# Optimization experiments

Hardware: AMD Instinct MI355X
Metric: run time of the kernel (lower is better)

## Reference

```python
import jax, jax.numpy as jnp
import numpy as np

B, T, DM = 4, 1024, 1024
H, NW = 16, 16
HD = DM // H  # 64


def _l2norm(x, eps=1e-12):
    n = jnp.sqrt(jnp.sum(x * x, axis=-1, keepdims=True))
    return x / jnp.maximum(n, eps)


def setup_inputs() -> dict:
    key = jax.random.key(0)
    ks = jax.random.split(key, 14)
    s = 0.02
    d = {
        "x": jax.random.normal(ks[0], (B, T, DM), jnp.float32),
        "Wqf": jax.random.normal(ks[1], (H * NW, DM), jnp.float32) * s,
        "bqf": jnp.zeros((H * NW,), jnp.float32),
        "Wkf": jax.random.normal(ks[2], (H * NW, DM), jnp.float32) * s,
        "bkf": jnp.zeros((H * NW,), jnp.float32),
        "Wqp": jax.random.normal(ks[3], (H * NW, DM), jnp.float32) * s,
        "bqp": jnp.zeros((H * NW,), jnp.float32),
        "Wkp": jax.random.normal(ks[4], (H * NW, DM), jnp.float32) * s,
        "bkp": jnp.zeros((H * NW,), jnp.float32),
        "Wv": jax.random.normal(ks[5], (DM, DM), jnp.float32) * s,
        "bv": jnp.zeros((DM,), jnp.float32),
        "Wo": jax.random.normal(ks[6], (DM, DM), jnp.float32) * s,
        "bo": jnp.zeros((DM,), jnp.float32),
        "inter_scale": jnp.ones((H, 1, 1), jnp.float32),
    }
    return d


def reference(x, Wqf, bqf, Wkf, bkf, Wqp, bqp, Wkp, bkp, Wv, bv, Wo, bo, inter_scale):
    b, t, c = x.shape
    # projections -> [b, H, t, NW]
    def proj(W, bb, w_last):
        return (x @ W.T + bb).reshape(b, t, H, w_last).transpose(0, 2, 1, 3)

    q_f = proj(Wqf, bqf, NW)
    k_f = proj(Wkf, bkf, NW)
    q_p = proj(Wqp, bqp, NW)
    k_p = proj(Wkp, bkp, NW)
    v = proj(Wv, bv, HD)  # [b,H,t,HD]

    t_pos = jnp.arange(t, dtype=x.dtype)[None, None, :, None]  # [1,1,t,1]
    q_waves = jnp.sin(q_f * t_pos + q_p)
    k_waves = jnp.sin(k_f * t_pos + k_p)

    scale_factor = NW ** 0.25
    q_norm = _l2norm(q_waves) * scale_factor
    k_norm = _l2norm(k_waves) * scale_factor

    # wave interference scores [b,H,t,t]
    interference = jnp.einsum('bhtw,bhsw->bhts', q_norm, k_norm)
    interference = interference * inter_scale  # broadcast [H,1,1]

    causal = jnp.tril(jnp.ones((t, t), dtype=bool))  # True = attended
    # elu_plus_one kernel; masked positions -> elu(-inf)+1 == 0
    attn = jnp.where(causal, jax.nn.elu(interference) + 1.0, 0.0)

    num_attended = jnp.arange(1, t + 1, dtype=x.dtype)[None, None, :, None]
    attn = attn / jnp.sqrt(num_attended)

    out = jnp.einsum('bhts,bhsd->bhtd', attn, v)  # [b,H,t,HD]
    out = out.transpose(0, 2, 1, 3).reshape(b, t, c)
    return out @ Wo.T + bo
```

## Files before the change

### kernel.cpp

```cpp
#include <hip/hip_runtime.h>
#include <math.h>

typedef __attribute__((ext_vector_type(8))) short bf16x8;
typedef __attribute__((ext_vector_type(4))) float f32x4;
typedef __attribute__((ext_vector_type(4))) int i32x4;

typedef __attribute__((address_space(3))) void lds_void;
typedef __attribute__((address_space(1))) const void glb_cvoid;

__device__ __forceinline__ unsigned short f32_to_bf16(float f) {
    unsigned u = __float_as_uint(f);
    unsigned r = (u + 0x7FFFu + ((u >> 16) & 1u)) >> 16;
    return (unsigned short)r;
}
__device__ __forceinline__ float bf16_to_f32(unsigned short h) {
    return __uint_as_float(((unsigned)h) << 16);
}

__global__ __launch_bounds__(256)
void split_bf16(const float* __restrict__ src, unsigned short* __restrict__ hi,
                unsigned short* __restrict__ lo, int n4)
{
    const int i = blockIdx.x * 256 + threadIdx.x;
    if (i >= n4) return;
    float4 v = *reinterpret_cast<const float4*>(src + (size_t)i * 4);
    ushort4 h;
    h.x = f32_to_bf16(v.x); h.y = f32_to_bf16(v.y);
    h.z = f32_to_bf16(v.z); h.w = f32_to_bf16(v.w);
    *reinterpret_cast<ushort4*>(hi + (size_t)i * 4) = h;
    if (lo) {
        ushort4 l;
        l.x = f32_to_bf16(v.x - bf16_to_f32(h.x));
        l.y = f32_to_bf16(v.y - bf16_to_f32(h.y));
        l.z = f32_to_bf16(v.z - bf16_to_f32(h.z));
        l.w = f32_to_bf16(v.w - bf16_to_f32(h.w));
        *reinterpret_cast<ushort4*>(lo + (size_t)i * 4) = l;
    }
}

__global__ __launch_bounds__(256)
void split4_bf16(const float* __restrict__ Wqf, const float* __restrict__ Wkf,
                 const float* __restrict__ Wqp, const float* __restrict__ Wkp,
                 unsigned short* __restrict__ WfH, unsigned short* __restrict__ WfL,
                 unsigned short* __restrict__ WpH)
{
    const int i = blockIdx.x * 256 + threadIdx.x;
    const int sel = i >> 16, j = i & 65535;
    const float* W = (sel == 0) ? Wqf : (sel == 1) ? Wkf : (sel == 2) ? Wqp : Wkp;
    float4 v = *reinterpret_cast<const float4*>(W + (size_t)j * 4);
    ushort4 h;
    h.x = f32_to_bf16(v.x); h.y = f32_to_bf16(v.y);
    h.z = f32_to_bf16(v.z); h.w = f32_to_bf16(v.w);
    const size_t o = (size_t)(sel & 1) * 262144 + (size_t)j * 4;
    if (sel < 2) {
        *reinterpret_cast<ushort4*>(WfH + o) = h;
        ushort4 l;
        l.x = f32_to_bf16(v.x - bf16_to_f32(h.x));
        l.y = f32_to_bf16(v.y - bf16_to_f32(h.y));
        l.z = f32_to_bf16(v.z - bf16_to_f32(h.z));
        l.w = f32_to_bf16(v.w - bf16_to_f32(h.w));
        *reinterpret_cast<ushort4*>(WfL + o) = l;
    } else {
        *reinterpret_cast<ushort4*>(WpH + o) = h;
    }
}

__device__ __forceinline__ void xcd_tiles(int& tm, int& tn) {
    const int L = blockIdx.x + gridDim.x * blockIdx.y;
    const int nbn = gridDim.x;
    const int q3 = L >> 3;
    tn = q3 % nbn;
    tm = (L & 7) + 8 * (q3 / nbn);
}

__global__ __launch_bounds__(256)
void freq_gemm_norm(const unsigned short* __restrict__ xh,
                    const unsigned short* __restrict__ xl,
                    const unsigned short* __restrict__ WfH,
                    const unsigned short* __restrict__ WfL,
                    const unsigned short* __restrict__ WpH,
                    const float* __restrict__ bqf, const float* __restrict__ bkf,
                    const float* __restrict__ bqp, const float* __restrict__ bkp,
                    unsigned short* __restrict__ qn, unsigned short* __restrict__ kn)
{
    __shared__ __attribute__((aligned(16))) unsigned short Al[32 * 64];
    __shared__ __attribute__((aligned(16))) unsigned short Bl[64 * 64];

    int tm, tn;
    xcd_tiles(tm, tn);
    const int bm = tm * 32, bn = tn * 64;

    const int tid = threadIdx.x;
    const int w = tid >> 6, l = tid & 63;
    const int wr = w >> 1, wc = w & 1;
    const int lr = l & 15, lg = l >> 4;
    const int r8 = l >> 3;
    const int c8 = l & 7;
    const int csw = (c8 ^ r8) << 3;

    f32x4 accF[2], accP[2];
#pragma unroll
    for (int j = 0; j < 2; j++)
#pragma unroll
        for (int r = 0; r < 4; r++) { accF[j][r] = 0.f; accP[j][r] = 0.f; }

    for (int t = 0; t < 64; ++t) {
        const int seg = t >> 4;
        const int kc = (t << 6) & 1023;
        const unsigned short* Aseg = (seg == 1) ? xl : xh;
        const unsigned short* Bseg = (seg <= 1) ? WfH : (seg == 2) ? WfL : WpH;

        __builtin_amdgcn_global_load_lds(
            (glb_cvoid*)(Aseg + (size_t)(bm + w * 8 + r8) * 1024 + kc + csw),
            (lds_void*)(&Al[(w * 8) * 64]), 16, 0, 0);
#pragma unroll
        for (int i = 0; i < 2; i++)
            __builtin_amdgcn_global_load_lds(
                (glb_cvoid*)(Bseg + (size_t)(bn + w * 16 + i * 8 + r8) * 1024 + kc + csw),
                (lds_void*)(&Bl[(w * 16 + i * 8) * 64]), 16, 0, 0);
        __syncthreads();

        bf16x8 af[2], bfr[2][2];
#pragma unroll
        for (int kk = 0; kk < 2; kk++) {
            af[kk] = *reinterpret_cast<const bf16x8*>(
                &Al[(wr * 16 + lr) * 64 + (((kk * 4 + lg) ^ (lr & 7)) << 3)]);
#pragma unroll
            for (int j = 0; j < 2; j++)
                bfr[j][kk] = *reinterpret_cast<const bf16x8*>(
                    &Bl[(wc * 32 + j * 16 + lr) * 64 + (((kk * 4 + lg) ^ (lr & 7)) << 3)]);
        }
        if (seg < 3) {
#pragma unroll
            for (int kk = 0; kk < 2; kk++)
#pragma unroll
                for (int j = 0; j < 2; j++)
                    accF[j] = __builtin_amdgcn_mfma_f32_16x16x32_bf16(
                        af[kk], bfr[j][kk], accF[j], 0, 0, 0);
        } else {
#pragma unroll
            for (int kk = 0; kk < 2; kk++)
#pragma unroll
                for (int j = 0; j < 2; j++)
                    accP[j] = __builtin_amdgcn_mfma_f32_16x16x32_bf16(
                        af[kk], bfr[j][kk], accP[j], 0, 0, 0);
        }
        __syncthreads();
    }

#pragma unroll
    for (int j = 0; j < 2; j++) {
        const int col = bn + wc * 32 + j * 16 + lr;
        const bool isQ = col < 256;
        const int c = col & 255;
        const float bf = isQ ? bqf[c] : bkf[c];
        const float bp = isQ ? bqp[c] : bkp[c];
        unsigned short* dst = isQ ? qn : kn;
        const int h = c >> 4, ww = c & 15;
#pragma unroll
        for (int r = 0; r < 4; r++) {
            const int row = bm + wr * 16 + lg * 4 + r;
            const int b = row >> 10, t = row & 1023;
            const float f = accF[j][r] + bf;
            const float p = accP[j][r] + bp;
            const float s = __sinf(fmaf(f, (float)t, p));
            float n2 = s * s;
#pragma unroll
            for (int off = 8; off >= 1; off >>= 1)
                n2 += __shfl_xor(n2, off);
            const float val = s * 2.0f / fmaxf(sqrtf(n2), 1e-12f);
            dst[((size_t)(b * 16 + h) * 1024 + t) * 16 + ww] = f32_to_bf16(val);
        }
    }
}

template <int MODE>
__global__ __launch_bounds__(256)
void mfma_gemm(const unsigned short* __restrict__ A0,
               const unsigned short* __restrict__ B0,
               const float* __restrict__ bias,
               float* __restrict__ outF, unsigned short* __restrict__ outH)
{
    __shared__ __attribute__((aligned(16))) unsigned short Al[64 * 64];
    __shared__ __attribute__((aligned(16))) unsigned short Bl[64 * 64];

    int tm, tn;
    xcd_tiles(tm, tn);
    const int bm = tm * 64, bn = tn * 64;

    const int tid = threadIdx.x;
    const int w = tid >> 6, l = tid & 63;
    const int wr = w >> 1, wc = w & 1;
    const int lr = l & 15, lg = l >> 4;
    const int r8 = l >> 3;
    const int c8 = l & 7;
    const int csw = (c8 ^ r8) << 3;

    f32x4 acc[2][2];
#pragma unroll
    for (int i = 0; i < 2; i++)
#pragma unroll
        for (int j = 0; j < 2; j++)
#pragma unroll
            for (int r = 0; r < 4; r++) acc[i][j][r] = 0.f;

    for (int t = 0; t < 16; ++t) {
        const int k0 = t << 6;
#pragma unroll
        for (int i = 0; i < 2; i++) {
            __builtin_amdgcn_global_load_lds(
                (glb_cvoid*)(A0 + (size_t)(bm + w * 16 + i * 8 + r8) * 1024 + k0 + csw),
                (lds_void*)(&Al[(w * 16 + i * 8) * 64]), 16, 0, 0);
            __builtin_amdgcn_global_load_lds(
                (glb_cvoid*)(B0 + (size_t)(bn + w * 16 + i * 8 + r8) * 1024 + k0 + csw),
                (lds_void*)(&Bl[(w * 16 + i * 8) * 64]), 16, 0, 0);
        }
        __syncthreads();

        bf16x8 af[2][2], bfr[2][2];
#pragma unroll
        for (int i = 0; i < 2; i++)
#pragma unroll
            for (int kk = 0; kk < 2; kk++) {
                af[i][kk] = *reinterpret_cast<const bf16x8*>(
                    &Al[(wr * 32 + i * 16 + lr) * 64 + (((kk * 4 + lg) ^ (lr & 7)) << 3)]);
                bfr[i][kk] = *reinterpret_cast<const bf16x8*>(
                    &Bl[(wc * 32 + i * 16 + lr) * 64 + (((kk * 4 + lg) ^ (lr & 7)) << 3)]);
            }
#pragma unroll
        for (int kk = 0; kk < 2; kk++)
#pragma unroll
            for (int i = 0; i < 2; i++)
#pragma unroll
                for (int j = 0; j < 2; j++)
                    acc[i][j] = __builtin_amdgcn_mfma_f32_16x16x32_bf16(
                        af[i][kk], bfr[j][kk], acc[i][j], 0, 0, 0);
        __syncthreads();
    }

#pragma unroll
    for (int i = 0; i < 2; i++) {
#pragma unroll
        for (int j = 0; j < 2; j++) {
#pragma unroll
            for (int r = 0; r < 4; r++) {
                const int row = bm + wr * 32 + i * 16 + lg * 4 + r;
                const int col = bn + wc * 32 + j * 16 + lr;
                float v = acc[i][j][r] + bias[col];
                if (MODE == 1) {
                    const int hh = col >> 6, d = col & 63;
                    const int b = row >> 10, t = row & 1023;
                    outH[(((size_t)(b * 16 + hh) * 64 + d) * 1024) + t] =
                        f32_to_bf16(v);
                } else {
                    outF[(size_t)row * 1024 + col] = v;
                }
            }
        }
    }
}

__global__ __launch_bounds__(512)
void wave_attn_mfma(const unsigned short* __restrict__ qn,
                    const unsigned short* __restrict__ kn,
                    const unsigned short* __restrict__ vtt,
                    const float* __restrict__ iscale,
                    unsigned short* __restrict__ y)
{
    const int p = blockIdx.x, bh = blockIdx.y;
    const int h = bh & 15, b = bh >> 4;
    const int tid = threadIdx.x;
    const int wq = tid >> 6;
    const int l = tid & 63;
    const int lt = l & 15;
    const int gl = l >> 4;
    const int it = (wq < 4) ? p : (15 - p);
    const int t0w = it * 64 + (wq & 3) * 16;
    const float scale = iscale[h];
    const int tmine = t0w + lt;

    const bf16x8 zero8 = {0, 0, 0, 0, 0, 0, 0, 0};
    const f32x4 zf = {0.f, 0.f, 0.f, 0.f};
    const size_t kb = (size_t)bh * 1024;

    bf16x8 bq = zero8;
    if (gl < 2)
        bq = *reinterpret_cast<const bf16x8*>(&qn[(kb + t0w + lt) * 16 + gl * 8]);

    f32x4 o[4];
#pragma unroll
    for (int jd = 0; jd < 4; jd++) o[jd] = zf;

    const int addr0 = ((2 * (gl & 1)) * 16 + lt) * 4;
    const int addr1 = addr0 + 64;
    const bool hi = ((gl >> 1) & 1) != 0;

    bf16x8 akc[4], akn[4];
#pragma unroll
    for (int js = 0; js < 4; js++) {
        akc[js] = zero8;
        if (gl < 2)
            akc[js] = *reinterpret_cast<const bf16x8*>(
                &kn[(kb + js * 16 + lt) * 16 + gl * 8]);
    }

    for (int is = 0; is <= it; is++) {
        const int s0 = is * 64;

        if (is < it) {
#pragma unroll
            for (int js = 0; js < 4; js++) {
                akn[js] = zero8;
                if (gl < 2)
                    akn[js] = *reinterpret_cast<const bf16x8*>(
                        &kn[(kb + s0 + 64 + js * 16 + lt) * 16 + gl * 8]);
            }
        }
        bf16x8 bv[2][4];
#pragma unroll
        for (int ks = 0; ks < 2; ks++)
#pragma unroll
            for (int jd = 0; jd < 4; jd++)
                bv[ks][jd] = *reinterpret_cast<const bf16x8*>(
                    &vtt[((size_t)(bh * 64 + jd * 16 + lt)) * 1024 +
                         s0 + ks * 32 + gl * 8]);

        f32x4 st[4];
#pragma unroll
        for (int js = 0; js < 4; js++)
            st[js] = __builtin_amdgcn_mfma_f32_16x16x32_bf16(
                akc[js], bq, zf, 0, 0, 0);

        int pk[4][2];
#pragma unroll
        for (int js = 0; js < 4; js++) {
            float pp[4];
#pragma unroll
            for (int r = 0; r < 4; r++) {
                const int s = s0 + js * 16 + gl * 4 + r;
                const float xv = st[js][r] * scale;
                const float phi = (xv > 0.f) ? (xv + 1.0f) : __expf(xv);
                pp[r] = (s <= tmine) ? phi : 0.f;
            }
            asm("v_cvt_pk_bf16_f32 %0, %1, %2"
                : "=v"(pk[js][0]) : "v"(pp[0]), "v"(pp[1]));
            asm("v_cvt_pk_bf16_f32 %0, %1, %2"
                : "=v"(pk[js][1]) : "v"(pp[2]), "v"(pp[3]));
        }

        int rg[4][2][2];
#pragma unroll
        for (int js = 0; js < 4; js++)
#pragma unroll
            for (int sl = 0; sl < 2; sl++) {
                rg[js][sl][0] = __builtin_amdgcn_ds_bpermute(addr0, pk[js][sl]);
                rg[js][sl][1] = __builtin_amdgcn_ds_bpermute(addr1, pk[js][sl]);
            }

#pragma unroll
        for (int ks = 0; ks < 2; ks++) {
            i32x4 au;
#pragma unroll
            for (int c = 0; c < 2; c++)
#pragma unroll
                for (int sl = 0; sl < 2; sl++)
                    au[2 * c + sl] = hi ? rg[2 * ks + 1][sl][c]
                                        : rg[2 * ks][sl][c];
            const bf16x8 pa = __builtin_bit_cast(bf16x8, au);
#pragma unroll
            for (int jd = 0; jd < 4; jd++)
                o[jd] = __builtin_amdgcn_mfma_f32_16x16x32_bf16(
                    pa, bv[ks][jd], o[jd], 0, 0, 0);
        }

#pragma unroll
        for (int js = 0; js < 4; js++) akc[js] = akn[js];
    }

#pragma unroll
    for (int r = 0; r < 4; r++) {
        const int t = t0w + gl * 4 + r;
        const float inv = rsqrtf((float)(t + 1));
#pragma unroll
        for (int jd = 0; jd < 4; jd++) {
            const int d = jd * 16 + lt;
            y[((size_t)b * 1024 + t) * 1024 + h * 64 + d] =
                f32_to_bf16(o[jd][r] * inv);
        }
    }
}

extern "C" void kernel_launch(void* const* d_in, const int* in_sizes, int n_in,
                              void* d_out, int out_size, void* d_ws, size_t ws_size,
                              hipStream_t stream)
{
    const float* x   = (const float*)d_in[0];
    const float* Wqf = (const float*)d_in[1];
    const float* bqf = (const float*)d_in[2];
    const float* Wkf = (const float*)d_in[3];
    const float* bkf = (const float*)d_in[4];
    const float* Wqp = (const float*)d_in[5];
    const float* bqp = (const float*)d_in[6];
    const float* Wkp = (const float*)d_in[7];
    const float* bkp = (const float*)d_in[8];
    const float* Wv  = (const float*)d_in[9];
    const float* bv  = (const float*)d_in[10];
    const float* Wo  = (const float*)d_in[11];
    const float* bo  = (const float*)d_in[12];
    const float* isc = (const float*)d_in[13];
    float* out = (float*)d_out;

    char* ws = (char*)d_ws;
    unsigned short* ybf = (unsigned short*)(ws);
    unsigned short* qn  = (unsigned short*)(ws + ( 8u << 20));
    unsigned short* kn  = (unsigned short*)(ws + (10u << 20));
    unsigned short* WfH = (unsigned short*)(ws + (12u << 20));
    unsigned short* WfL = (unsigned short*)(ws + (13u << 20));
    unsigned short* WpH = (unsigned short*)(ws + (14u << 20));
    unsigned short* xh  = (unsigned short*)(ws + (16u << 20));
    unsigned short* xl  = (unsigned short*)(ws + (24u << 20));
    unsigned short* vtt = (unsigned short*)(ws + (24u << 20));
    unsigned short* WvH = (unsigned short*)(ws + (32u << 20));
    unsigned short* WoH = WvH;

    split_bf16<<<4096, 256, 0, stream>>>(x, xh, xl, 1048576);
    split4_bf16<<<1024, 256, 0, stream>>>(Wqf, Wkf, Wqp, Wkp, WfH, WfL, WpH);

    freq_gemm_norm<<<dim3(8, 128), 256, 0, stream>>>(
        xh, xl, WfH, WfL, WpH, bqf, bkf, bqp, bkp, qn, kn);

    split_bf16<<<1024, 256, 0, stream>>>(Wv, WvH, nullptr, 262144);
    mfma_gemm<1><<<dim3(16, 64), 256, 0, stream>>>(xh, WvH, bv, nullptr, vtt);

    wave_attn_mfma<<<dim3(8, 64), 512, 0, stream>>>(qn, kn, vtt, isc, ybf);

    split_bf16<<<1024, 256, 0, stream>>>(Wo, WoH, nullptr, 262144);
    mfma_gemm<2><<<dim3(16, 64), 256, 0, stream>>>(ybf, WoH, bo, out, nullptr);
}
```

Before: 220.3 us.

## Load GEMM operands directly from global into registers and merge Wv/Wo conversion

Both GEMM kernels drop LDS staging (global_load_lds plus barriers) and have each lane read its MFMA fragments straight from global memory. Operands that were shared through LDS are now re-read per wave and served by the caches. This removes the barriers and LDS traffic but makes global loads uncoalesced, with 16-byte strided rows. Separately, the Wv and Wo bf16 conversions become one kernel launched early, which needs a separate WoH buffer.

```diff
diff --git a/kernel.cpp b/kernel.cpp
--- a/kernel.cpp
+++ b/kernel.cpp
@@ -4,9 +4,6 @@
 typedef __attribute__((ext_vector_type(8))) short bf16x8;
 typedef __attribute__((ext_vector_type(4))) float f32x4;
 typedef __attribute__((ext_vector_type(4))) int i32x4;
-
-typedef __attribute__((address_space(3))) void lds_void;
-typedef __attribute__((address_space(1))) const void glb_cvoid;
 
 __device__ __forceinline__ unsigned short f32_to_bf16(float f) {
     unsigned u = __float_as_uint(f);
@@ -65,6 +62,21 @@
     }
 }
 
+__global__ __launch_bounds__(256)
+void splitW2_bf16(const float* __restrict__ Wv, const float* __restrict__ Wo,
+                  unsigned short* __restrict__ WvH, unsigned short* __restrict__ WoH)
+{
+    const int i = blockIdx.x * 256 + threadIdx.x;
+    const int sel = i >> 18, j = i & 262143;
+    const float* W = sel ? Wo : Wv;
+    unsigned short* D = sel ? WoH : WvH;
+    float4 v = *reinterpret_cast<const float4*>(W + (size_t)j * 4);
+    ushort4 h;
+    h.x = f32_to_bf16(v.x); h.y = f32_to_bf16(v.y);
+    h.z = f32_to_bf16(v.z); h.w = f32_to_bf16(v.w);
+    *reinterpret_cast<ushort4*>(D + (size_t)j * 4) = h;
+}
+
 __device__ __forceinline__ void xcd_tiles(int& tm, int& tn) {
     const int L = blockIdx.x + gridDim.x * blockIdx.y;
     const int nbn = gridDim.x;
@@ -83,9 +95,6 @@
                     const float* __restrict__ bqp, const float* __restrict__ bkp,
                     unsigned short* __restrict__ qn, unsigned short* __restrict__ kn)
 {
-    __shared__ __attribute__((aligned(16))) unsigned short Al[32 * 64];
-    __shared__ __attribute__((aligned(16))) unsigned short Bl[64 * 64];
-
     int tm, tn;
     xcd_tiles(tm, tn);
     const int bm = tm * 32, bn = tn * 64;
@@ -94,9 +103,10 @@
     const int w = tid >> 6, l = tid & 63;
     const int wr = w >> 1, wc = w & 1;
     const int lr = l & 15, lg = l >> 4;
-    const int r8 = l >> 3;
-    const int c8 = l & 7;
-    const int csw = (c8 ^ r8) << 3;
+
+    const size_t aoff  = (size_t)(bm + wr * 16 + lr) * 1024 + lg * 8;
+    const size_t boff0 = (size_t)(bn + wc * 32 + lr) * 1024 + lg * 8;
+    const size_t boff1 = boff0 + 16 * 1024;
 
     f32x4 accF[2], accP[2];
 #pragma unroll
@@ -104,49 +114,26 @@
 #pragma unroll
         for (int r = 0; r < 4; r++) { accF[j][r] = 0.f; accP[j][r] = 0.f; }
 
-    for (int t = 0; t < 64; ++t) {
-        const int seg = t >> 4;
-        const int kc = (t << 6) & 1023;
-        const unsigned short* Aseg = (seg == 1) ? xl : xh;
-        const unsigned short* Bseg = (seg <= 1) ? WfH : (seg == 2) ? WfL : WpH;
-
-        __builtin_amdgcn_global_load_lds(
-            (glb_cvoid*)(Aseg + (size_t)(bm + w * 8 + r8) * 1024 + kc + csw),
-            (lds_void*)(&Al[(w * 8) * 64]), 16, 0, 0);
-#pragma unroll
-        for (int i = 0; i < 2; i++)
-            __builtin_amdgcn_global_load_lds(
-                (glb_cvoid*)(Bseg + (size_t)(bn + w * 16 + i * 8 + r8) * 1024 + kc + csw),
-                (lds_void*)(&Bl[(w * 16 + i * 8) * 64]), 16, 0, 0);
-        __syncthreads();
-
-        bf16x8 af[2], bfr[2][2];
-#pragma unroll
-        for (int kk = 0; kk < 2; kk++) {
-            af[kk] = *reinterpret_cast<const bf16x8*>(
-                &Al[(wr * 16 + lr) * 64 + (((kk * 4 + lg) ^ (lr & 7)) << 3)]);
-#pragma unroll
-            for (int j = 0; j < 2; j++)
-                bfr[j][kk] = *reinterpret_cast<const bf16x8*>(
-                    &Bl[(wc * 32 + j * 16 + lr) * 64 + (((kk * 4 + lg) ^ (lr & 7)) << 3)]);
-        }
-        if (seg < 3) {
-#pragma unroll
-            for (int kk = 0; kk < 2; kk++)
-#pragma unroll
-                for (int j = 0; j < 2; j++)
-                    accF[j] = __builtin_amdgcn_mfma_f32_16x16x32_bf16(
-                        af[kk], bfr[j][kk], accF[j], 0, 0, 0);
-        } else {
-#pragma unroll
-            for (int kk = 0; kk < 2; kk++)
-#pragma unroll
-                for (int j = 0; j < 2; j++)
-                    accP[j] = __builtin_amdgcn_mfma_f32_16x16x32_bf16(
-                        af[kk], bfr[j][kk], accP[j], 0, 0, 0);
-        }
-        __syncthreads();
-    }
+    auto run_seg = [&](const unsigned short* __restrict__ A,
+                       const unsigned short* __restrict__ B, f32x4* acc) {
+#pragma unroll 4
+        for (int t = 0; t < 16; ++t) {
+            const int kc = t << 6;
+#pragma unroll
+            for (int kk = 0; kk < 2; kk++) {
+                const int ko = kc + kk * 32;
+                bf16x8 a  = *reinterpret_cast<const bf16x8*>(A + aoff  + ko);
+                bf16x8 b0 = *reinterpret_cast<const bf16x8*>(B + boff0 + ko);
+                bf16x8 b1 = *reinterpret_cast<const bf16x8*>(B + boff1 + ko);
+                acc[0] = __builtin_amdgcn_mfma_f32_16x16x32_bf16(a, b0, acc[0], 0, 0, 0);
+                acc[1] = __builtin_amdgcn_mfma_f32_16x16x32_bf16(a, b1, acc[1], 0, 0, 0);
+            }
+        }
+    };
+    run_seg(xh, WfH, accF);
+    run_seg(xl, WfH, accF);
+    run_seg(xh, WfL, accF);
+    run_seg(xh, WpH, accP);
 
 #pragma unroll
     for (int j = 0; j < 2; j++) {
@@ -181,9 +168,6 @@
                const float* __restrict__ bias,
                float* __restrict__ outF, unsigned short* __restrict__ outH)
 {
-    __shared__ __attribute__((aligned(16))) unsigned short Al[64 * 64];
-    __shared__ __attribute__((aligned(16))) unsigned short Bl[64 * 64];
-
     int tm, tn;
     xcd_tiles(tm, tn);
     const int bm = tm * 64, bn = tn * 64;
@@ -192,9 +176,11 @@
     const int w = tid >> 6, l = tid & 63;
     const int wr = w >> 1, wc = w & 1;
     const int lr = l & 15, lg = l >> 4;
-    const int r8 = l >> 3;
-    const int c8 = l & 7;
-    const int csw = (c8 ^ r8) << 3;
+
+    const size_t a0off = (size_t)(bm + wr * 32 + lr) * 1024 + lg * 8;
+    const size_t a1off = a0off + 16 * 1024;
+    const size_t b0off = (size_t)(bn + wc * 32 + lr) * 1024 + lg * 8;
+    const size_t b1off = b0off + 16 * 1024;
 
     f32x4 acc[2][2];
 #pragma unroll
@@ -204,38 +190,21 @@
 #pragma unroll
             for (int r = 0; r < 4; r++) acc[i][j][r] = 0.f;
 
+#pragma unroll 2
     for (int t = 0; t < 16; ++t) {
-        const int k0 = t << 6;
-#pragma unroll
-        for (int i = 0; i < 2; i++) {
-            __builtin_amdgcn_global_load_lds(
-                (glb_cvoid*)(A0 + (size_t)(bm + w * 16 + i * 8 + r8) * 1024 + k0 + csw),
-                (lds_void*)(&Al[(w * 16 + i * 8) * 64]), 16, 0, 0);
-            __builtin_amdgcn_global_load_lds(
-                (glb_cvoid*)(B0 + (size_t)(bn + w * 16 + i * 8 + r8) * 1024 + k0 + csw),
-                (lds_void*)(&Bl[(w * 16 + i * 8) * 64]), 16, 0, 0);
-        }
-        __syncthreads();
-
-        bf16x8 af[2][2], bfr[2][2];
-#pragma unroll
-        for (int i = 0; i < 2; i++)
-#pragma unroll
-            for (int kk = 0; kk < 2; kk++) {
-                af[i][kk] = *reinterpret_cast<const bf16x8*>(
-                    &Al[(wr * 32 + i * 16 + lr) * 64 + (((kk * 4 + lg) ^ (lr & 7)) << 3)]);
-                bfr[i][kk] = *reinterpret_cast<const bf16x8*>(
-                    &Bl[(wc * 32 + i * 16 + lr) * 64 + (((kk * 4 + lg) ^ (lr & 7)) << 3)]);
-            }
-#pragma unroll
-        for (int kk = 0; kk < 2; kk++)
-#pragma unroll
-            for (int i = 0; i < 2; i++)
-#pragma unroll
-                for (int j = 0; j < 2; j++)
-                    acc[i][j] = __builtin_amdgcn_mfma_f32_16x16x32_bf16(
-                        af[i][kk], bfr[j][kk], acc[i][j], 0, 0, 0);
-        __syncthreads();
+        const int kc = t << 6;
+#pragma unroll
+        for (int kk = 0; kk < 2; kk++) {
+            const int ko = kc + kk * 32;
+            bf16x8 a0 = *reinterpret_cast<const bf16x8*>(A0 + a0off + ko);
+            bf16x8 a1 = *reinterpret_cast<const bf16x8*>(A0 + a1off + ko);
+            bf16x8 b0 = *reinterpret_cast<const bf16x8*>(B0 + b0off + ko);
+            bf16x8 b1 = *reinterpret_cast<const bf16x8*>(B0 + b1off + ko);
+            acc[0][0] = __builtin_amdgcn_mfma_f32_16x16x32_bf16(a0, b0, acc[0][0], 0, 0, 0);
+            acc[0][1] = __builtin_amdgcn_mfma_f32_16x16x32_bf16(a0, b1, acc[0][1], 0, 0, 0);
+            acc[1][0] = __builtin_amdgcn_mfma_f32_16x16x32_bf16(a1, b0, acc[1][0], 0, 0, 0);
+            acc[1][1] = __builtin_amdgcn_mfma_f32_16x16x32_bf16(a1, b1, acc[1][1], 0, 0, 0);
+        }
     }
 
 #pragma unroll
@@ -421,19 +390,18 @@
     unsigned short* xl  = (unsigned short*)(ws + (24u << 20));
     unsigned short* vtt = (unsigned short*)(ws + (24u << 20));
     unsigned short* WvH = (unsigned short*)(ws + (32u << 20));
-    unsigned short* WoH = WvH;
+    unsigned short* WoH = (unsigned short*)(ws + (34u << 20));
 
     split_bf16<<<4096, 256, 0, stream>>>(x, xh, xl, 1048576);
     split4_bf16<<<1024, 256, 0, stream>>>(Wqf, Wkf, Wqp, Wkp, WfH, WfL, WpH);
+    splitW2_bf16<<<2048, 256, 0, stream>>>(Wv, Wo, WvH, WoH);
 
     freq_gemm_norm<<<dim3(8, 128), 256, 0, stream>>>(
         xh, xl, WfH, WfL, WpH, bqf, bkf, bqp, bkp, qn, kn);
 
-    split_bf16<<<1024, 256, 0, stream>>>(Wv, WvH, nullptr, 262144);
     mfma_gemm<1><<<dim3(16, 64), 256, 0, stream>>>(xh, WvH, bv, nullptr, vtt);
 
     wave_attn_mfma<<<dim3(8, 64), 512, 0, stream>>>(qn, kn, vtt, isc, ybf);
 
-    split_bf16<<<1024, 256, 0, stream>>>(Wo, WoH, nullptr, 262144);
     mfma_gemm<2><<<dim3(16, 64), 256, 0, stream>>>(ybf, WoH, bo, out, nullptr);
 }
```

New measurement: 431.9 us. 1.96x slower.
